# Kernel tuning notes

Hardware: AMD Instinct MI355X
Metric: run time of the kernel (lower is better)

## Reference

```python
import jax, jax.numpy as jnp
import numpy as np

N_HEAD = 16
D_HEAD = 64
LN_EPS = 1e-5


def _layernorm(x, g, b):
    mu = jnp.mean(x, axis=-1, keepdims=True)
    var = jnp.mean((x - mu) ** 2, axis=-1, keepdims=True)
    return (x - mu) * jax.lax.rsqrt(var + LN_EPS) * g + b


def setup_inputs() -> dict:
    key = jax.random.key(0)
    ks = jax.random.split(key, 10)
    n_token, d_model, d_inner, n_layer = 32000, 1024, 4096, 6
    qlen, mlen, bsz = 512, 512, 4
    s = 0.02
    return {
        'data': jax.random.randint(ks[0], (qlen, bsz), 0, n_token),
        'mems': jax.random.normal(ks[1], (n_layer, mlen, bsz, d_model), jnp.float32) * s,
        'emb': jax.random.normal(ks[2], (n_token, d_model), jnp.float32) * s,
        'Wq': jax.random.normal(ks[3], (n_layer, d_model, N_HEAD * D_HEAD), jnp.float32) * s,
        'Wkv': jax.random.normal(ks[4], (n_layer, d_model, 2 * N_HEAD * D_HEAD), jnp.float32) * s,
        'Wo': jax.random.normal(ks[5], (n_layer, N_HEAD * D_HEAD, d_model), jnp.float32) * s,
        'ln1_g': jnp.ones((n_layer, d_model), jnp.float32),
        'ln1_b': jnp.zeros((n_layer, d_model), jnp.float32),
        'W1': jax.random.normal(ks[6], (n_layer, d_model, d_inner), jnp.float32) * s,
        'b1': jnp.zeros((n_layer, d_inner), jnp.float32),
        'W2': jax.random.normal(ks[7], (n_layer, d_inner, d_model), jnp.float32) * s,
        'b2': jnp.zeros((n_layer, d_model), jnp.float32),
        'ln2_g': jnp.ones((n_layer, d_model), jnp.float32),
        'ln2_b': jnp.zeros((n_layer, d_model), jnp.float32),
    }


def reference(data, mems, emb, Wq, Wkv, Wo, ln1_g, ln1_b, W1, b1, W2, b2, ln2_g, ln2_b):
    qlen, bsz = data.shape
    n_layer, _, d_model = Wo.shape
    mlen = mems.shape[1]
    klen = mlen + qlen
    scale = 1.0 / np.sqrt(D_HEAD)

    # AdaptiveEmbedding (div_val=1, d_proj==d_embed): lookup * sqrt(d_proj)
    word_emb = emb[data] * np.sqrt(d_model)  # [q, b, d]

    # sinusoidal positional embedding over klen (attn_type=2), last qlen slice
    inv_freq = 1.0 / (10000.0 ** (jnp.arange(0, d_model, 2, dtype=jnp.float32) / d_model))
    pos_seq = jnp.arange(klen - 1, -1, -1, dtype=jnp.float32)
    sinu = pos_seq[:, None] * inv_freq[None, :]
    pos_emb = jnp.concatenate([jnp.sin(sinu), jnp.cos(sinu)], axis=-1)  # [klen, d]
    h = word_emb + pos_emb[-qlen:, None, :]

    # causal mask including memory: True = masked
    mask = jnp.triu(jnp.ones((qlen, klen), dtype=bool), k=1 + mlen)

    for l in range(n_layer):
        c = jnp.concatenate([mems[l], h], axis=0)  # [klen, b, d]
        q = (h @ Wq[l]).reshape(qlen, bsz, N_HEAD, D_HEAD)
        kv = (c @ Wkv[l]).reshape(klen, bsz, N_HEAD, 2 * D_HEAD)
        k, v = kv[..., :D_HEAD], kv[..., D_HEAD:]
        score = jnp.einsum('ibnd,jbnd->ijbn', q, k) * scale  # [q, klen, b, n]
        score = jnp.where(mask[:, :, None, None], -jnp.inf, score)
        prob = jax.nn.softmax(score, axis=1)
        attn_vec = jnp.einsum('ijbn,jbnd->ibnd', prob, v).reshape(qlen, bsz, N_HEAD * D_HEAD)
        h = _layernorm(h + attn_vec @ Wo[l], ln1_g[l], ln1_b[l])  # post-LN
        ff = jax.nn.relu(h @ W1[l] + b1[l]) @ W2[l] + b2[l]
        h = _layernorm(h + ff, ln2_g[l], ln2_b[l])
    return h
```

## Files before the change

kernel.cpp:

```cpp
#include <hip/hip_runtime.h>

typedef unsigned short u16;
typedef unsigned int u32;
typedef __bf16 bf16x8 __attribute__((ext_vector_type(8)));
typedef float f32x4 __attribute__((ext_vector_type(4)));
typedef u16 u16x8 __attribute__((ext_vector_type(8)));
typedef u16 u16x4 __attribute__((ext_vector_type(4)));
typedef u32 u32x4 __attribute__((ext_vector_type(4)));

__device__ __forceinline__ u16 f2bf(float f){
  unsigned u = __float_as_uint(f);
  u += 0x7FFFu + ((u >> 16) & 1u);
  return (u16)(u >> 16);
}
__device__ __forceinline__ float bf2f(u16 u){
  return __uint_as_float((u32)u << 16);
}
__device__ __forceinline__ u32 pack2bf(float a, float b){
  return (u32)f2bf(a) | ((u32)f2bf(b) << 16);
}
__device__ __forceinline__ void gload16(const void* g, void* l){
  __builtin_amdgcn_global_load_lds(
      (const __attribute__((address_space(1))) void*)g,
      (__attribute__((address_space(3))) void*)l, 16, 0, 0);
}

__global__ __launch_bounds__(256) void conv_bf16_t(const float* __restrict__ src, u16* __restrict__ dst,
                                                   int K, int N, size_t dls, int drow0){
  __shared__ u16 s[64 * 68];
  size_t lo = (size_t)blockIdx.z * K * N;
  int n0 = blockIdx.x << 6, k0 = blockIdx.y << 6;
  int t = threadIdx.x;
#pragma unroll
  for (int p = 0; p < 4; ++p){
    int idx = p * 1024 + t * 4;
    int kl = idx >> 6, nl = idx & 63;
    f32x4 v = *(const f32x4*)(src + lo + (size_t)(k0 + kl) * N + n0 + nl);
#pragma unroll
    for (int j = 0; j < 4; ++j) s[(nl + j) * 68 + kl] = f2bf(v[j]);
  }
  __syncthreads();
  u16* db = dst + blockIdx.z * dls;
#pragma unroll
  for (int p = 0; p < 4; ++p){
    int idx = p * 1024 + t * 4;
    int nl = idx >> 6, kl = idx & 63;
    u16x4 o;
#pragma unroll
    for (int j = 0; j < 4; ++j) o[j] = s[nl * 68 + kl + j];
    *(u16x4*)(db + (size_t)(drow0 + n0 + nl) * K + k0 + kl) = o;
  }
}

__global__ __launch_bounds__(256) void conv_bf16(const float* __restrict__ src, u16* __restrict__ dst){
  size_t i = ((size_t)blockIdx.x * 256 + threadIdx.x) * 4;
  f32x4 v = *(const f32x4*)(src + i);
  u16x4 o;
#pragma unroll
  for (int j = 0; j < 4; ++j) o[j] = f2bf(v[j]);
  *(u16x4*)(dst + i) = o;
}

__global__ __launch_bounds__(256) void embed_k(const int* __restrict__ data, const float* __restrict__ emb,
                                               u16* __restrict__ hbf){
  int idx = blockIdx.x * 256 + threadIdx.x;
  int r = idx >> 10, d = idx & 1023;
  int i = r >> 2;
  int e = data[r];
  float val = emb[(size_t)e * 1024 + d] * 32.0f;
  float pos = (float)(511 - i);
  int t = d & 511;
  float freq = powf(10000.0f, -(float)t * (1.0f / 512.0f));
  float ang = pos * freq;
  val += (d < 512) ? sinf(ang) : cosf(ang);
  hbf[idx] = f2bf(val);
}

template<int BM>
__global__ __launch_bounds__(256) void gemm_bt(
    const u16* __restrict__ A, const u16* __restrict__ Bt,
    const float* __restrict__ bias, float* __restrict__ C, u16* __restrict__ Cbf,
    u16* __restrict__ Cpart, int M, int N, int K, int kchunk, int relu,
    size_t zA, size_t zB, size_t zC,
    u16* __restrict__ VT, size_t zVT, int vcol0, int jdst0)
{
  constexpr int MFR = BM / 32;
  constexpr int ASZ = BM * 64, BSZ = 128 * 64;
  __shared__ __align__(16) u16 sA[2 * ASZ];
  __shared__ __align__(16) u16 sB[2 * BSZ];
  int tid = threadIdx.x, lane = tid & 63;
  int wr = (tid >> 7) & 1, wc = (tid >> 6) & 1;
  int m0 = blockIdx.y * BM, n0 = blockIdx.x << 7;
  int z = blockIdx.z;
  int kbeg = Cpart ? z * kchunk : 0;

  const u16* Ap = A + (size_t)z * zA;
  const u16* Bp = Bt + (size_t)z * zB;

  f32x4 acc[MFR][4];
#pragma unroll
  for (int i = 0; i < MFR; ++i)
#pragma unroll
    for (int j = 0; j < 4; ++j) acc[i][j] = (f32x4)(0.0f);

  int srow8 = tid >> 3;
  int gslot8 = ((tid & 7) ^ (srow8 & 7)) << 3;
  const u16* Ab = Ap + (size_t)(m0 + srow8) * K + kbeg + gslot8;
  const u16* Bb = Bp + (size_t)(n0 + srow8) * K + kbeg + gslot8;
  const size_t rstep32 = (size_t)K << 5;

  auto stage = [&](int buf, int k0){
#pragma unroll
    for (int p = 0; p < BM / 32; ++p)
      gload16(Ab + p * rstep32 + k0, (void*)&sA[buf * ASZ + p * 2048 + tid * 8]);
#pragma unroll
    for (int p = 0; p < 4; ++p)
      gload16(Bb + p * rstep32 + k0, (void*)&sB[buf * BSZ + p * 2048 + tid * 8]);
  };

  int r15 = lane & 15, g = lane >> 4;
  int s0 = g ^ (r15 & 7);
  const int o0 = s0 * 8, o1 = (s0 ^ 4) * 8;
  const int paBase = (wr * (BM / 2) + r15) * 64;
  const int pbBase = (wc * 64 + r15) * 64;

  int nk = kchunk >> 6;
  stage(0, 0);
  __syncthreads();
  for (int t = 0; t < nk; ++t){
    int cur = t & 1;
    if (t + 1 < nk) stage(cur ^ 1, (t + 1) << 6);
    const u16* pa = sA + cur * ASZ;
    const u16* pb = sB + cur * BSZ;
    bf16x8 af[MFR][2], bfv[4][2];
#pragma unroll
    for (int mi = 0; mi < MFR; ++mi){
      af[mi][0] = *(const bf16x8*)(pa + paBase + mi * 1024 + o0);
      af[mi][1] = *(const bf16x8*)(pa + paBase + mi * 1024 + o1);
    }
#pragma unroll
    for (int ni = 0; ni < 4; ++ni){
      bfv[ni][0] = *(const bf16x8*)(pb + pbBase + ni * 1024 + o0);
      bfv[ni][1] = *(const bf16x8*)(pb + pbBase + ni * 1024 + o1);
    }
#pragma unroll
    for (int kk = 0; kk < 2; ++kk)
#pragma unroll
      for (int mi = 0; mi < MFR; ++mi)
#pragma unroll
        for (int ni = 0; ni < 4; ++ni)
          acc[mi][ni] = __builtin_amdgcn_mfma_f32_16x16x32_bf16(af[mi][kk], bfv[ni][kk], acc[mi][ni], 0, 0, 0);
    __syncthreads();
  }

  int colf = lane & 15, rowf = (lane >> 4) << 2;
  bool vtile = (VT != nullptr) && (n0 >= vcol0);
  if (Cpart){
    u16* dst = Cpart + (size_t)z * M * N;
#pragma unroll
    for (int ni = 0; ni < 4; ++ni){
      int cg = n0 + (wc << 6) + ni * 16 + colf;
#pragma unroll
      for (int mi = 0; mi < MFR; ++mi){
        int rg = m0 + wr * (BM / 2) + mi * 16 + rowf;
#pragma unroll
        for (int r = 0; r < 4; ++r)
          dst[(size_t)(rg + r) * N + cg] = f2bf(acc[mi][ni][r]);
      }
    }
  } else {
    if (!(vtile && wc == 1)){
#pragma unroll
      for (int ni = 0; ni < 4; ++ni){
        int cg = n0 + (wc << 6) + ni * 16 + colf;
        float bv = bias ? bias[cg] : 0.0f;
#pragma unroll
        for (int mi = 0; mi < MFR; ++mi){
          int rg = m0 + wr * (BM / 2) + mi * 16 + rowf;
#pragma unroll
          for (int r = 0; r < 4; ++r){
            float val = acc[mi][ni][r] + bv;
            if (relu) val = fmaxf(val, 0.0f);
            size_t o = (size_t)(rg + r) * N + cg;
            if (C)   C[o]   = val;
            if (Cbf) (Cbf + (size_t)z * zC)[o] = f2bf(val);
          }
        }
      }
    }
    if (vtile){
      if (wc == 1){
#pragma unroll
        for (int ni = 0; ni < 4; ++ni)
#pragma unroll
          for (int mi = 0; mi < MFR; ++mi)
#pragma unroll
            for (int r = 0; r < 4; ++r)
              sA[(wr * (BM / 2) + mi * 16 + rowf + r) * 68 + ni * 16 + colf] = f2bf(acc[mi][ni][r]);
      }
      __syncthreads();
      int vb = tid >> 6, vd = tid & 63;
      int nh = (n0 - vcol0) >> 7;
      u16* dst = VT + (size_t)z * zVT + (((size_t)((vb << 4) + nh) << 6) + vd) * 1024 + jdst0 + (m0 >> 2);
      u16 tmp[BM / 4];
#pragma unroll
      for (int jj = 0; jj < BM / 4; ++jj) tmp[jj] = sA[((jj << 2) + vb) * 68 + vd];
#pragma unroll
      for (int c = 0; c < BM / 32; ++c)
        *(u16x8*)(dst + c * 8) = *(const u16x8*)(&tmp[c * 8]);
    }
  }
}

__global__ __launch_bounds__(256) void attn_mfma(
    const u16* __restrict__ qkv, const u16* __restrict__ kvm,
    const u16* __restrict__ vtbf, u16* __restrict__ attnbf)
{
  __shared__ __align__(16) u16 sK[4][64 * 64];
  __shared__ __align__(16) u16 sV[4][64 * 64];
  int tid = threadIdx.x, lane = tid & 63, wid = tid >> 6;
  int g = lane >> 4, t = lane & 15;
  int qt = blockIdx.x, bnp = blockIdx.y;
  int b = bnp >> 4, n = bnp & 15;
  int i0 = qt * 64 + wid * 16;
  int i = i0 + t;

  union Cvt { u32x4 u; bf16x8 v; };

  bf16x8 qfrag[2];
#pragma unroll
  for (int ks = 0; ks < 2; ++ks)
    qfrag[ks] = *(const bf16x8*)(qkv + (size_t)(i * 4 + b) * 3072 + n * 64 + ks * 32 + g * 8);

  f32x4 oacc[4];
#pragma unroll
  for (int df = 0; df < 4; ++df) oacc[df] = (f32x4)(0.0f);
  float mrun = -1e30f, lrun = 0.0f;

  const u16* kbm = kvm + n * 128;
  const u16* kbh = qkv + 1024 + n * 128;
  const u16* vb2 = vtbf + ((size_t)bnp << 16);

  int srow = tid >> 3;
  int gsl = ((tid & 7) ^ (srow & 7)) << 3;

  auto stageKV = [&](int buf, int kt){
    int j0 = kt << 6;
    const u16* kb = (kt < 8) ? kbm : kbh;
    size_t kst = (kt < 8) ? 2048 : 3072;
    int joff = (kt < 8) ? 0 : 512;
#pragma unroll
    for (int p = 0; p < 2; ++p){
      int jl = srow + p * 32;
      gload16(kb + (size_t)((j0 + jl - joff) * 4 + b) * kst + gsl, (void*)&sK[buf][p * 2048 + tid * 8]);
    }
#pragma unroll
    for (int p = 0; p < 2; ++p){
      int dl = srow + p * 32;
      gload16(vb2 + ((size_t)dl << 10) + j0 + gsl, (void*)&sV[buf][p * 2048 + tid * 8]);
    }
  };

  auto compute = [&](int cur, int kt){
    int j0 = kt << 6;
    f32x4 sacc[4];
#pragma unroll
    for (int jf = 0; jf < 4; ++jf) sacc[jf] = (f32x4)(0.0f);
    __builtin_amdgcn_s_setprio(1);
#pragma unroll
    for (int ks = 0; ks < 2; ++ks){
      int sl = ((ks * 4 + g) ^ (t & 7)) * 8;
#pragma unroll
      for (int jf = 0; jf < 4; ++jf){
        bf16x8 kf = *(const bf16x8*)(&sK[cur][(jf * 16 + t) * 64 + sl]);
        sacc[jf] = __builtin_amdgcn_mfma_f32_16x16x32_bf16(kf, qfrag[ks], sacc[jf], 0, 0, 0);
      }
    }
    __builtin_amdgcn_s_setprio(0);
    bool part = (j0 + 63 > i0 + 512);
    float ps[4][4];
    float tmax = -1e30f;
#pragma unroll
    for (int jf = 0; jf < 4; ++jf)
#pragma unroll
      for (int r = 0; r < 4; ++r){
        float s = sacc[jf][r] * 0.125f;
        if (part && (j0 + jf * 16 + g * 4 + r > i + 512)) s = -1e30f;
        ps[jf][r] = s;
        tmax = fmaxf(tmax, s);
      }
    tmax = fmaxf(tmax, __shfl_xor(tmax, 16));
    tmax = fmaxf(tmax, __shfl_xor(tmax, 32));
    float mnew = fmaxf(mrun, tmax);
    float sc = __expf(mrun - mnew);
    mrun = mnew;
    lrun *= sc;
    u32 pk0[2], pk1[2], pk2[2], pk3[2];
    {
      float e0, e1, e2, e3;
#define DO_JF(PK, JF) \
      e0 = __expf(ps[JF][0] - mnew); e1 = __expf(ps[JF][1] - mnew); \
      e2 = __expf(ps[JF][2] - mnew); e3 = __expf(ps[JF][3] - mnew); \
      lrun += (e0 + e1) + (e2 + e3); \
      PK[0] = pack2bf(e0, e1); PK[1] = pack2bf(e2, e3);
      DO_JF(pk0, 0) DO_JF(pk1, 1) DO_JF(pk2, 2) DO_JF(pk3, 3)
#undef DO_JF
    }
#pragma unroll
    for (int df = 0; df < 4; ++df)
#pragma unroll
      for (int r = 0; r < 4; ++r) oacc[df][r] *= sc;

    int srcA = t + 16 * ((2 * g) & 3);
    int srcB = t + 16 * ((2 * g + 1) & 3);
    bool ghi = (g >= 2);
#pragma unroll
    for (int ks = 0; ks < 2; ++ks){
      u32 w0a, w1a, w2a, w3a, w0b, w1b, w2b, w3b;
      if (ks == 0){
        w0a = __shfl((int)pk0[0], srcA); w1a = __shfl((int)pk0[1], srcA);
        w2a = __shfl((int)pk0[0], srcB); w3a = __shfl((int)pk0[1], srcB);
        w0b = __shfl((int)pk1[0], srcA); w1b = __shfl((int)pk1[1], srcA);
        w2b = __shfl((int)pk1[0], srcB); w3b = __shfl((int)pk1[1], srcB);
      } else {
        w0a = __shfl((int)pk2[0], srcA); w1a = __shfl((int)pk2[1], srcA);
        w2a = __shfl((int)pk2[0], srcB); w3a = __shfl((int)pk2[1], srcB);
        w0b = __shfl((int)pk3[0], srcA); w1b = __shfl((int)pk3[1], srcA);
        w2b = __shfl((int)pk3[0], srcB); w3b = __shfl((int)pk3[1], srcB);
      }
      Cvt c;
      c.u[0] = ghi ? w0b : w0a;
      c.u[1] = ghi ? w1b : w1a;
      c.u[2] = ghi ? w2b : w2a;
      c.u[3] = ghi ? w3b : w3a;
      bf16x8 pf = c.v;
      int sl = ((ks * 4 + g) ^ (t & 7)) * 8;
      __builtin_amdgcn_s_setprio(1);
#pragma unroll
      for (int df = 0; df < 4; ++df){
        bf16x8 vf = *(const bf16x8*)(&sV[cur][(df * 16 + t) * 64 + sl]);
        oacc[df] = __builtin_amdgcn_mfma_f32_16x16x32_bf16(vf, pf, oacc[df], 0, 0, 0);
      }
      __builtin_amdgcn_s_setprio(0);
    }
  };

  int kt1 = qt + 9;
  stageKV(0, 0);
  stageKV(1, 1);
  __syncthreads();
  for (int kt = 0; kt < kt1; kt += 2){
    if (kt + 2 < kt1) stageKV((kt + 2) & 3, kt + 2);
    if (kt + 3 < kt1) stageKV((kt + 3) & 3, kt + 3);
    compute(kt & 3, kt);
    if (kt + 1 < kt1) compute((kt + 1) & 3, kt + 1);
    __syncthreads();
  }
  lrun += __shfl_xor(lrun, 16);
  lrun += __shfl_xor(lrun, 32);
  float inv = 1.0f / lrun;

  u16* orow = attnbf + ((size_t)(i * 4 + b) << 10) + n * 64;
#pragma unroll
  for (int df = 0; df < 4; ++df){
#pragma unroll
    for (int h = 0; h < 2; ++h){
      *(u32*)(orow + df * 16 + g * 4 + 2 * h) = pack2bf(oacc[df][2 * h] * inv, oacc[df][2 * h + 1] * inv);
    }
  }
}

__global__ __launch_bounds__(256) void ln_k(const u16* __restrict__ resbf, const u16* __restrict__ parts,
                                            size_t pstride, int np, const float* __restrict__ bias,
                                            const float* __restrict__ g, const float* __restrict__ bta,
                                            u16* __restrict__ hbf, float* __restrict__ fout)
{
  int row = blockIdx.x, tid = threadIdx.x;
  int d0 = tid << 2;
  size_t ro = (size_t)row << 10;
  u16x4 rv = *(const u16x4*)(resbf + ro + d0);
  f32x4 v;
#pragma unroll
  for (int j = 0; j < 4; ++j) v[j] = bf2f(rv[j]);
  if (bias){
    f32x4 bv = *(const f32x4*)(bias + d0);
#pragma unroll
    for (int j = 0; j < 4; ++j) v[j] += bv[j];
  }
  for (int p = 0; p < np; ++p){
    u16x4 pv = *(const u16x4*)(parts + p * pstride + ro + d0);
#pragma unroll
    for (int j = 0; j < 4; ++j) v[j] += bf2f(pv[j]);
  }
  float s = (v[0] + v[1]) + (v[2] + v[3]);
  float s2 = (v[0] * v[0] + v[1] * v[1]) + (v[2] * v[2] + v[3] * v[3]);
#pragma unroll
  for (int off = 32; off; off >>= 1){ s += __shfl_xor(s, off); s2 += __shfl_xor(s2, off); }
  __shared__ float ps[8];
  int wid = tid >> 6, lane = tid & 63;
  if (lane == 0){ ps[wid] = s; ps[wid + 4] = s2; }
  __syncthreads();
  s  = ps[0] + ps[1] + ps[2] + ps[3];
  s2 = ps[4] + ps[5] + ps[6] + ps[7];
  float mu = s * 0.0009765625f;
  float var = s2 * 0.0009765625f - mu * mu;
  float rstd = rsqrtf(var + 1e-5f);
  f32x4 gv = *(const f32x4*)(g + d0);
  f32x4 bt = *(const f32x4*)(bta + d0);
  f32x4 fo;
  u16x4 hb;
#pragma unroll
  for (int j = 0; j < 4; ++j){
    float tv = (v[j] - mu) * rstd * gv[j] + bt[j];
    fo[j] = tv; hb[j] = f2bf(tv);
  }
  *(u16x4*)(hbf + ro + d0) = hb;
  if (fout) *(f32x4*)(fout + ro + d0) = fo;
}

extern "C" void kernel_launch(void* const* d_in, const int* in_sizes, int n_in,
                              void* d_out, int out_size, void* d_ws, size_t ws_size,
                              hipStream_t stream)
{
  const int*   data = (const int*)  d_in[0];
  const float* mems = (const float*)d_in[1];
  const float* emb  = (const float*)d_in[2];
  const float* Wq   = (const float*)d_in[3];
  const float* Wkv  = (const float*)d_in[4];
  const float* Wo   = (const float*)d_in[5];
  const float* ln1g = (const float*)d_in[6];
  const float* ln1b = (const float*)d_in[7];
  const float* W1   = (const float*)d_in[8];
  const float* b1   = (const float*)d_in[9];
  const float* W2   = (const float*)d_in[10];
  const float* b2   = (const float*)d_in[11];
  const float* ln2g = (const float*)d_in[12];
  const float* ln2b = (const float*)d_in[13];
  float* out = (float*)d_out;

  char* ws = (char*)d_ws;
  size_t off = 0;
  auto alloc = [&](size_t bytes) -> char* {
    char* p = ws + off;
    off = (off + bytes + 255) & ~(size_t)255;
    return p;
  };

  u16*   wqkv_bf = (u16*) alloc((size_t)6 * 3072 * 1024 * 2);
  u16*   wo_bf   = (u16*) alloc((size_t)6 * 1024 * 1024 * 2);
  u16*   w1_bf   = (u16*) alloc((size_t)6 * 4096 * 1024 * 2);
  u16*   w2_bf   = (u16*) alloc((size_t)6 * 1024 * 4096 * 2);
  u16*   memsbf  = (u16*) alloc((size_t)6 * 2048 * 1024 * 2);
  u16*   kvmem   = (u16*) alloc((size_t)6 * 2048 * 2048 * 2);
  u16*   vtbf    = (u16*) alloc((size_t)6 * 64 * 64 * 1024 * 2);
  u16*   hbf     = (u16*) alloc((size_t)2048 * 1024 * 2);
  u16*   qkv     = (u16*) alloc((size_t)2048 * 3072 * 2);
  u16*   attnbf  = (u16*) alloc((size_t)2048 * 1024 * 2);
  u16*   f1bf    = (u16*) alloc((size_t)2048 * 4096 * 2);
  u16*   pbf     = (u16*) alloc((size_t)4 * 2048 * 1024 * 2);
  const size_t PS = (size_t)2048 * 1024;
  const size_t VTL = (size_t)64 * 64 * 1024;

  conv_bf16_t<<<dim3(16, 16, 6), 256, 0, stream>>>(Wq,  wqkv_bf, 1024, 1024, (size_t)3072 * 1024, 0);
  conv_bf16_t<<<dim3(32, 16, 6), 256, 0, stream>>>(Wkv, wqkv_bf, 1024, 2048, (size_t)3072 * 1024, 1024);
  conv_bf16_t<<<dim3(16, 16, 6), 256, 0, stream>>>(Wo,  wo_bf,   1024, 1024, (size_t)1024 * 1024, 0);
  conv_bf16_t<<<dim3(64, 16, 6), 256, 0, stream>>>(W1,  w1_bf,   1024, 4096, (size_t)4096 * 1024, 0);
  conv_bf16_t<<<dim3(16, 64, 6), 256, 0, stream>>>(W2,  w2_bf,   4096, 1024, (size_t)4096 * 1024, 0);
  conv_bf16<<<12288, 256, 0, stream>>>(mems, memsbf);
  embed_k<<<8192, 256, 0, stream>>>(data, emb, hbf);
  gemm_bt<128><<<dim3(16, 16, 6), 256, 0, stream>>>(memsbf, wqkv_bf + (size_t)1024 * 1024, nullptr,
      nullptr, kvmem, nullptr, 2048, 2048, 1024, 1024, 0,
      (size_t)2048 * 1024, (size_t)3072 * 1024, (size_t)2048 * 2048,
      vtbf, VTL, 0, 0);

  for (int l = 0; l < 6; ++l){
    u16* kvm_l = kvmem + (size_t)l * 2048 * 2048;
    u16* vt_l  = vtbf + (size_t)l * VTL;
    gemm_bt<64><<<dim3(24, 32), 256, 0, stream>>>(hbf, wqkv_bf + (size_t)l * 3072 * 1024, nullptr,
        nullptr, qkv, nullptr, 2048, 3072, 1024, 1024, 0, 0, 0, 0,
        vt_l, 0, 1024, 512);
    attn_mfma<<<dim3(8, 64), 256, 0, stream>>>(qkv, kvm_l, vt_l, attnbf);
    gemm_bt<64><<<dim3(8, 32, 2), 256, 0, stream>>>(attnbf, wo_bf + (size_t)l * 1024 * 1024, nullptr,
        nullptr, nullptr, pbf, 2048, 1024, 1024, 512, 0, 0, 0, 0,
        nullptr, 0, 0, 0);
    ln_k<<<2048, 256, 0, stream>>>(hbf, pbf, PS, 2, nullptr, ln1g + l * 1024, ln1b + l * 1024, hbf, nullptr);
    gemm_bt<128><<<dim3(32, 16), 256, 0, stream>>>(hbf, w1_bf + (size_t)l * 4096 * 1024,
        b1 + (size_t)l * 4096, nullptr, f1bf, nullptr, 2048, 4096, 1024, 1024, 1, 0, 0, 0,
        nullptr, 0, 0, 0);
    gemm_bt<128><<<dim3(8, 16, 4), 256, 0, stream>>>(f1bf, w2_bf + (size_t)l * 4096 * 1024, nullptr,
        nullptr, nullptr, pbf, 2048, 1024, 4096, 1024, 0, 0, 0, 0,
        nullptr, 0, 0, 0);
    ln_k<<<2048, 256, 0, stream>>>(hbf, pbf, PS, 4, b2 + l * 1024, ln2g + l * 1024, ln2b + l * 1024,
                                   hbf, (l == 5) ? out : nullptr);
  }
}
```

Before: 1.037 ms.

## Add 8-wave ping-pong GEMM kernel for FFN1 with bias and ReLU

Adds a new 512-thread GEMM kernel using 128x256 tiles, double-buffered direct-to-LDS loads with an XOR swizzle, and barrier-separated phases with s_setprio. Wave groups alternate between LDS fragment reads and MFMA bursts. The kernel replaces the previous 256-thread gemm_bt<128> for the W1 projection, with bias and ReLU fused in the epilogue. The goal is better MFMA utilisation and overlap of global loads with compute, at the cost of fewer blocks (256 on a 256-CU part) and a scalar, uncoalesced bf16 epilogue store.

```diff
diff --git a/kernel.cpp b/kernel.cpp
--- a/kernel.cpp
+++ b/kernel.cpp
@@ -208,6 +208,133 @@
 #pragma unroll
       for (int c = 0; c < BM / 32; ++c)
         *(u16x8*)(dst + c * 8) = *(const u16x8*)(&tmp[c * 8]);
+    }
+  }
+}
+
+__global__ __launch_bounds__(512) void gemm8ph(
+    const u16* __restrict__ A, const u16* __restrict__ Bt,
+    const float* __restrict__ bias, u16* __restrict__ Cbf,
+    int N, int K, int relu)
+{
+  __shared__ __align__(16) u16 sA[2][128 * 64];
+  __shared__ __align__(16) u16 sB[2][256 * 64];
+  int tid = threadIdx.x, lane = tid & 63, wid = tid >> 6;
+  int wr = wid >> 2, wc = wid & 3;
+  int m0 = blockIdx.y << 7, n0 = blockIdx.x << 8;
+
+  f32x4 acc[4][4];
+#pragma unroll
+  for (int i = 0; i < 4; ++i)
+#pragma unroll
+    for (int j = 0; j < 4; ++j) acc[i][j] = (f32x4)(0.0f);
+
+  int srow = tid >> 3;
+  int gslot = ((tid & 7) ^ (srow & 7)) << 3;
+  const u16* Ab = A + (size_t)(m0 + srow) * K + gslot;
+  const u16* Bb = Bt + (size_t)(n0 + srow) * K + gslot;
+  const size_t r64 = (size_t)K << 6;
+
+  auto stage = [&](int buf, int kt){
+    int k0 = kt << 6;
+    gload16(Ab + k0,            (void*)&sA[buf][tid * 8]);
+    gload16(Ab + r64 + k0,      (void*)&sA[buf][4096 + tid * 8]);
+    gload16(Bb + k0,            (void*)&sB[buf][tid * 8]);
+    gload16(Bb + r64 + k0,      (void*)&sB[buf][4096 + tid * 8]);
+    gload16(Bb + 2 * r64 + k0,  (void*)&sB[buf][8192 + tid * 8]);
+    gload16(Bb + 3 * r64 + k0,  (void*)&sB[buf][12288 + tid * 8]);
+  };
+
+  int r15 = lane & 15, g = lane >> 4;
+  int s0 = g ^ (r15 & 7);
+  const int o0 = s0 * 8, o1 = (s0 ^ 4) * 8;
+  const int aRow = wr * 64 + r15;
+  const int bRow = wc * 64 + r15;
+
+  int nu = K >> 6;
+  stage(0, 0);
+  asm volatile("s_waitcnt vmcnt(0)" ::: "memory");
+  __builtin_amdgcn_s_barrier();
+
+  for (int u = 0; u < nu; ++u){
+    int cb = u & 1;
+    const u16* pa = &sA[cb][0];
+    const u16* pb = &sB[cb][0];
+    bf16x8 bf[4], af[2];
+    if (u + 1 < nu) stage(cb ^ 1, u + 1);
+#pragma unroll
+    for (int ni = 0; ni < 4; ++ni) bf[ni] = *(const bf16x8*)(pb + (bRow + ni * 16) * 64 + o0);
+    af[0] = *(const bf16x8*)(pa + (aRow + 0) * 64 + o0);
+    af[1] = *(const bf16x8*)(pa + (aRow + 16) * 64 + o0);
+    __builtin_amdgcn_s_barrier();
+    asm volatile("s_waitcnt lgkmcnt(0)" ::: "memory");
+    __builtin_amdgcn_sched_barrier(0);
+    __builtin_amdgcn_s_setprio(1);
+#pragma unroll
+    for (int ni = 0; ni < 4; ++ni){
+      acc[0][ni] = __builtin_amdgcn_mfma_f32_16x16x32_bf16(af[0], bf[ni], acc[0][ni], 0, 0, 0);
+      acc[1][ni] = __builtin_amdgcn_mfma_f32_16x16x32_bf16(af[1], bf[ni], acc[1][ni], 0, 0, 0);
+    }
+    __builtin_amdgcn_s_setprio(0);
+    __builtin_amdgcn_s_barrier();
+    af[0] = *(const bf16x8*)(pa + (aRow + 32) * 64 + o0);
+    af[1] = *(const bf16x8*)(pa + (aRow + 48) * 64 + o0);
+    __builtin_amdgcn_s_barrier();
+    asm volatile("s_waitcnt lgkmcnt(0)" ::: "memory");
+    __builtin_amdgcn_sched_barrier(0);
+    __builtin_amdgcn_s_setprio(1);
+#pragma unroll
+    for (int ni = 0; ni < 4; ++ni){
+      acc[2][ni] = __builtin_amdgcn_mfma_f32_16x16x32_bf16(af[0], bf[ni], acc[2][ni], 0, 0, 0);
+      acc[3][ni] = __builtin_amdgcn_mfma_f32_16x16x32_bf16(af[1], bf[ni], acc[3][ni], 0, 0, 0);
+    }
+    __builtin_amdgcn_s_setprio(0);
+    __builtin_amdgcn_s_barrier();
+#pragma unroll
+    for (int ni = 0; ni < 4; ++ni) bf[ni] = *(const bf16x8*)(pb + (bRow + ni * 16) * 64 + o1);
+    af[0] = *(const bf16x8*)(pa + (aRow + 0) * 64 + o1);
+    af[1] = *(const bf16x8*)(pa + (aRow + 16) * 64 + o1);
+    __builtin_amdgcn_s_barrier();
+    asm volatile("s_waitcnt lgkmcnt(0)" ::: "memory");
+    __builtin_amdgcn_sched_barrier(0);
+    __builtin_amdgcn_s_setprio(1);
+#pragma unroll
+    for (int ni = 0; ni < 4; ++ni){
+      acc[0][ni] = __builtin_amdgcn_mfma_f32_16x16x32_bf16(af[0], bf[ni], acc[0][ni], 0, 0, 0);
+      acc[1][ni] = __builtin_amdgcn_mfma_f32_16x16x32_bf16(af[1], bf[ni], acc[1][ni], 0, 0, 0);
+    }
+    __builtin_amdgcn_s_setprio(0);
+    __builtin_amdgcn_s_barrier();
+    af[0] = *(const bf16x8*)(pa + (aRow + 32) * 64 + o1);
+    af[1] = *(const bf16x8*)(pa + (aRow + 48) * 64 + o1);
+    __builtin_amdgcn_s_barrier();
+    asm volatile("s_waitcnt lgkmcnt(0)" ::: "memory");
+    __builtin_amdgcn_sched_barrier(0);
+    __builtin_amdgcn_s_setprio(1);
+#pragma unroll
+    for (int ni = 0; ni < 4; ++ni){
+      acc[2][ni] = __builtin_amdgcn_mfma_f32_16x16x32_bf16(af[0], bf[ni], acc[2][ni], 0, 0, 0);
+      acc[3][ni] = __builtin_amdgcn_mfma_f32_16x16x32_bf16(af[1], bf[ni], acc[3][ni], 0, 0, 0);
+    }
+    __builtin_amdgcn_s_setprio(0);
+    asm volatile("s_waitcnt vmcnt(0)" ::: "memory");
+    __builtin_amdgcn_s_barrier();
+  }
+
+  int colf = lane & 15, rowf = (lane >> 4) << 2;
+#pragma unroll
+  for (int ni = 0; ni < 4; ++ni){
+    int cg = n0 + wc * 64 + ni * 16 + colf;
+    float bv = bias ? bias[cg] : 0.0f;
+#pragma unroll
+    for (int mi = 0; mi < 4; ++mi){
+      int rg = m0 + wr * 64 + mi * 16 + rowf;
+#pragma unroll
+      for (int r = 0; r < 4; ++r){
+        float val = acc[mi][ni][r] + bv;
+        if (relu) val = fmaxf(val, 0.0f);
+        Cbf[(size_t)(rg + r) * N + cg] = f2bf(val);
+      }
     }
   }
 }
@@ -484,9 +611,8 @@
         nullptr, nullptr, pbf, 2048, 1024, 1024, 512, 0, 0, 0, 0,
         nullptr, 0, 0, 0);
     ln_k<<<2048, 256, 0, stream>>>(hbf, pbf, PS, 2, nullptr, ln1g + l * 1024, ln1b + l * 1024, hbf, nullptr);
-    gemm_bt<128><<<dim3(32, 16), 256, 0, stream>>>(hbf, w1_bf + (size_t)l * 4096 * 1024,
-        b1 + (size_t)l * 4096, nullptr, f1bf, nullptr, 2048, 4096, 1024, 1024, 1, 0, 0, 0,
-        nullptr, 0, 0, 0);
+    gemm8ph<<<dim3(16, 16), 512, 0, stream>>>(hbf, w1_bf + (size_t)l * 4096 * 1024,
+        b1 + (size_t)l * 4096, f1bf, 4096, 1024, 1);
     gemm_bt<128><<<dim3(8, 16, 4), 256, 0, stream>>>(f1bf, w2_bf + (size_t)l * 4096 * 1024, nullptr,
         nullptr, nullptr, pbf, 2048, 1024, 4096, 1024, 0, 0, 0, 0,
         nullptr, 0, 0, 0);
```

After: 1.080 ms. +4.2%, slower.
